# Performance work log

Measured on AMD Instinct MI355X. Metric: run time of the kernel, lower is better.

## Reference

```python
import jax, jax.numpy as jnp
import numpy as np

B, C, H, W = 4, 256, 64, 64
CH = C // 2


def setup_inputs() -> dict:
    key = jax.random.key(0)
    ks = jax.random.split(key, 8)
    s_in = 1.0 / np.sqrt(C)  # conv2d default init scale (fan_in = C for 1x1)
    return {
        "a": jax.random.normal(ks[0], (B, C, H, W), dtype=jnp.float32),
        "p": jax.random.normal(ks[1], (B, C, H, W), dtype=jnp.float32),
        "Wq": jax.random.uniform(ks[2], (CH, C), jnp.float32, -s_in, s_in),
        "bq": jax.random.uniform(ks[3], (CH,), jnp.float32, -s_in, s_in),
        "Wk": jax.random.uniform(ks[4], (CH, C), jnp.float32, -s_in, s_in),
        "bk": jax.random.uniform(ks[5], (CH,), jnp.float32, -s_in, s_in),
        "Wv": jax.random.uniform(ks[6], (C, C), jnp.float32, -s_in, s_in),
        "bv": jax.random.uniform(ks[7], (C,), jnp.float32, -s_in, s_in),
    }


def reference(a, p, Wq, bq, Wk, bk, Wv, bv):
    b, c, h, w = a.shape
    hw = h * w
    # 1x1 convs == per-pixel channel matmuls; flatten spatial dims to hw
    Q = jnp.einsum('oc,bchw->bohw', Wq, a).reshape(b, -1, hw) + bq[None, :, None]   # [B, C/2, HW]
    K = jnp.einsum('oc,bchw->bohw', Wk, p).reshape(b, -1, hw) + bk[None, :, None]   # [B, C/2, HW]
    V = jnp.einsum('oc,bchw->bohw', Wv, p).reshape(b, -1, hw) + bv[None, :, None]   # [B, C,   HW]
    # attn[b,m,n] = softmax_n( Q[:, :, m] . K[:, :, n] )
    attn = jax.nn.softmax(jnp.einsum('bcm,bcn->bmn', Q, K), axis=-1)                # [B, HW, HW]
    # out[b,c,m] = sum_n V[b,c,n] * attn[b,m,n]  (V @ attn^T)
    out = jnp.einsum('bcn,bmn->bcm', V, attn).reshape(b, c, h, w)
    return out + a
```

## Files before the change

kernel.cpp:

```cpp
#include <hip/hip_runtime.h>
#include <stdint.h>

#define B_ 4
#define C_ 256
#define CH_ 128
#define HW_ 4096
#define L2E 1.44269504f
#define SHIFT_L2 14.4269504f

typedef __bf16 bf16;
typedef __bf16 v8bf __attribute__((ext_vector_type(8)));
typedef __bf16 v4bf __attribute__((ext_vector_type(4)));
typedef float v4f __attribute__((ext_vector_type(4)));
struct f4 { float x, y, z, w; };
struct f2 { float x, y; };

#define GAS __attribute__((address_space(1)))
#define LAS __attribute__((address_space(3)))

__device__ __forceinline__ void async_copy16(const void* gptr, void* lptr) {
  __builtin_amdgcn_global_load_lds((GAS void*)gptr, (LAS void*)lptr, 16, 0, 0);
}

__global__ __launch_bounds__(512)
void proj_kernel(const float* __restrict__ a, const float* __restrict__ p,
                 const float* __restrict__ Wq, const float* __restrict__ bq,
                 const float* __restrict__ Wk, const float* __restrict__ bk,
                 const float* __restrict__ Wv, const float* __restrict__ bv,
                 bf16* __restrict__ Qt, bf16* __restrict__ Kt, bf16* __restrict__ Vn)
{
  __shared__ bf16 Xt[64 * 272];
  __shared__ bf16 Ds[9216];

  const int t = threadIdx.x;
  const int lane = t & 63;
  const int w = t >> 6;
  const int l15 = lane & 15;
  const int q = lane >> 4;

  const int s0 = blockIdx.x * 64;
  const int b = blockIdx.y;
  const int z = blockIdx.z;

  const float* X = (z == 0) ? a : p;
  const float* Xb = X + ((size_t)b * C_) * HW_;
  #pragma unroll
  for (int j = 0; j < 8; ++j) {
    int linear = t + 512 * j;
    int s = (linear & 31) * 2;
    int cp = linear >> 5;
    f2 x0 = *(const f2*)&Xb[(size_t)(2 * cp) * HW_ + s0 + s];
    f2 x1 = *(const f2*)&Xb[(size_t)(2 * cp + 1) * HW_ + s0 + s];
    unsigned short u00 = __builtin_bit_cast(unsigned short, (bf16)x0.x);
    unsigned short u01 = __builtin_bit_cast(unsigned short, (bf16)x0.y);
    unsigned short u10 = __builtin_bit_cast(unsigned short, (bf16)x1.x);
    unsigned short u11 = __builtin_bit_cast(unsigned short, (bf16)x1.y);
    *(unsigned int*)&Xt[(s + 0) * 272 + 2 * cp] = (unsigned int)u00 | ((unsigned int)u10 << 16);
    *(unsigned int*)&Xt[(s + 1) * 272 + 2 * cp] = (unsigned int)u01 | ((unsigned int)u11 << 16);
  }

  __syncthreads();

  const int npass = (z == 0) ? 1 : 3;
  for (int pp = 0; pp < npass; ++pp) {
    const float* W; const float* bias;
    if (z == 0)      { W = Wq; bias = bq; }
    else if (pp == 0){ W = Wk; bias = bk; }
    else             { W = Wv + (size_t)(pp - 1) * 128 * C_; bias = bv + (pp - 1) * 128; }

    v8bf Af[8];
    const float* Wrow = W + (size_t)(16 * w + l15) * C_;
    #pragma unroll
    for (int kk = 0; kk < 8; ++kk) {
      f4 f0 = *(const f4*)&Wrow[kk * 32 + q * 8];
      f4 f1 = *(const f4*)&Wrow[kk * 32 + q * 8 + 4];
      v8bf f;
      f[0] = (bf16)f0.x; f[1] = (bf16)f0.y; f[2] = (bf16)f0.z; f[3] = (bf16)f0.w;
      f[4] = (bf16)f1.x; f[5] = (bf16)f1.y; f[6] = (bf16)f1.z; f[7] = (bf16)f1.w;
      Af[kk] = f;
    }

    v4f acc[4];
    #pragma unroll
    for (int ns = 0; ns < 4; ++ns) { v4f zz = {0.f, 0.f, 0.f, 0.f}; acc[ns] = zz; }
    #pragma unroll
    for (int ns = 0; ns < 4; ++ns)
      #pragma unroll
      for (int kk = 0; kk < 8; ++kk) {
        v8bf Bf = *(const v8bf*)&Xt[(16 * ns + l15) * 272 + kk * 32 + q * 8];
        acc[ns] = __builtin_amdgcn_mfma_f32_16x16x32_bf16(Af[kk], Bf, acc[ns], 0, 0, 0);
      }

    if (z == 0 || pp == 0) {
      #pragma unroll
      for (int ns = 0; ns < 4; ++ns)
        #pragma unroll
        for (int r = 0; r < 4; ++r)
          Ds[(16 * ns + l15) * 144 + 16 * w + 4 * q + r] =
              (bf16)(acc[ns][r] + bias[16 * w + 4 * q + r]);
      __syncthreads();
      bf16* dst = (z == 0) ? Qt : Kt;
      #pragma unroll
      for (int i = 0; i < 2; ++i) {
        int idx = t + 512 * i;
        int s = idx >> 4, ch = (idx & 15) * 8;
        *(v8bf*)&dst[((size_t)b * HW_ + s0 + s) * CH_ + ch] = *(const v8bf*)&Ds[s * 144 + ch];
      }
    } else {
      int o0 = (pp - 1) * 128;
      #pragma unroll
      for (int ns = 0; ns < 4; ++ns)
        #pragma unroll
        for (int r = 0; r < 4; ++r) {
          int pos = 32 * (ns >> 1) + 8 * (l15 >> 2) + 4 * (ns & 1) + (l15 & 3);
          Ds[(16 * w + 4 * q + r) * 72 + pos] =
              (bf16)(acc[ns][r] + bias[16 * w + 4 * q + r]);
        }
      __syncthreads();
      #pragma unroll
      for (int i = 0; i < 2; ++i) {
        int idx = t + 512 * i;
        int o = idx >> 3, ch = (idx & 7) * 8;
        *(v8bf*)&Vn[((size_t)b * C_ + o0 + o) * HW_ + s0 + ch] = *(const v8bf*)&Ds[o * 72 + ch];
      }
    }
    if (pp + 1 < npass) __syncthreads();
  }
}

#define LDS_V 16640
#define TSTRIDE 52
#define TREGION 13312
#define LDS_TOTAL 53248

__global__ __launch_bounds__(256, 2)
void attn_kernel(const bf16* __restrict__ Qt, const bf16* __restrict__ Kt,
                 const bf16* __restrict__ Vn, const float* __restrict__ a,
                 float* __restrict__ out, bf16* __restrict__ Op,
                 float* __restrict__ Ls, int nsplit)
{
  extern __shared__ char smem[];
  const int t = threadIdx.x;
  const int lane = t & 63;
  const int w = t >> 6;
  const int l15 = lane & 15;
  const int q = lane >> 4;
  const int b = blockIdx.y;
  const int sp = blockIdx.z;
  const int m0 = blockIdx.x * 128;

  v8bf Qf[2][4];
  #pragma unroll
  for (int s = 0; s < 2; ++s) {
    const bf16* qrow = Qt + ((size_t)b * HW_ + m0 + 32 * w + 16 * s + l15) * CH_;
    #pragma unroll
    for (int kk = 0; kk < 4; ++kk)
      Qf[s][kk] = *(const v8bf*)&qrow[kk * 32 + q * 8];
  }

  v4f O[2][16];
  #pragma unroll
  for (int s = 0; s < 2; ++s)
    #pragma unroll
    for (int cs = 0; cs < 16; ++cs) { v4f zz = {0.f, 0.f, 0.f, 0.f}; O[s][cs] = zz; }
  float lsum[2] = {0.f, 0.f};

  const bf16* Kb = Kt + (size_t)b * HW_ * CH_;
  const bf16* Vb = Vn + (size_t)b * C_ * HW_;

  const int NT = 64 / nsplit;
  const int t0 = sp * NT;

  auto stageK = [&](int n0) {
    #pragma unroll
    for (int j = 0; j < 4; ++j) {
      int i = 4 * j + w;
      async_copy16(Kb + ((size_t)(n0 + i + 16 * q)) * CH_ + l15 * 8, smem + i * 1040);
    }
  };
  auto stageV = [&](int n0) {
    #pragma unroll
    for (int j = 0; j < 8; ++j) {
      int i = 4 * j + w;
      async_copy16(Vb + ((size_t)(i + 32 * (lane >> 3))) * HW_ + n0 + (lane & 7) * 8,
                   smem + LDS_V + i * 1040);
    }
  };

  stageK(t0 * 64);
  stageV(t0 * 64);
  __syncthreads();

  for (int nt = 0; nt < NT; ++nt) {
    int n0 = (t0 + nt) * 64;

    v4f St[4][2];
    #pragma unroll
    for (int sub = 0; sub < 4; ++sub)
      #pragma unroll
      for (int s = 0; s < 2; ++s) { v4f zz = {0.f, 0.f, 0.f, 0.f}; St[sub][s] = zz; }
    #pragma unroll
    for (int sub = 0; sub < 4; ++sub)
      #pragma unroll
      for (int kk = 0; kk < 4; ++kk) {
        v8bf Kf = *(const v8bf*)(smem + l15 * 1040 + sub * 256 + kk * 64 + q * 16);
        St[sub][0] = __builtin_amdgcn_mfma_f32_16x16x32_bf16(Kf, Qf[0][kk], St[sub][0], 0, 0, 0);
        St[sub][1] = __builtin_amdgcn_mfma_f32_16x16x32_bf16(Kf, Qf[1][kk], St[sub][1], 0, 0, 0);
      }

    __syncthreads();
    if (nt + 1 < NT) stageK(n0 + 64);

    v8bf Pf[2][2];
    #pragma unroll
    for (int s = 0; s < 2; ++s) {
      float ls = 0.f;
      #pragma unroll
      for (int kk = 0; kk < 2; ++kk)
        #pragma unroll
        for (int a2 = 0; a2 < 2; ++a2)
          #pragma unroll
          for (int r = 0; r < 4; ++r) {
            float pv = exp2f(St[2 * kk + a2][s][r] * L2E - SHIFT_L2);
            Pf[s][kk][4 * a2 + r] = (bf16)pv;
            ls += pv;
          }
      lsum[s] += ls;
    }

    #pragma unroll
    for (int cs = 0; cs < 16; ++cs)
      #pragma unroll
      for (int kk = 0; kk < 2; ++kk) {
        v8bf Vf = *(const v8bf*)(smem + LDS_V +
                                 (16 * (cs & 1) + l15) * 1040 + (cs >> 1) * 128 + kk * 64 + q * 16);
        O[0][cs] = __builtin_amdgcn_mfma_f32_16x16x32_bf16(Pf[0][kk], Vf, O[0][cs], 0, 0, 0);
        O[1][cs] = __builtin_amdgcn_mfma_f32_16x16x32_bf16(Pf[1][kk], Vf, O[1][cs], 0, 0, 0);
      }

    __syncthreads();
    if (nt + 1 < NT) stageV(n0 + 64);
  }

  float lfin[2];
  #pragma unroll
  for (int s = 0; s < 2; ++s) {
    float l = lsum[s];
    l += __shfl_xor(l, 16);
    l += __shfl_xor(l, 32);
    lfin[s] = l;
  }

  if (nsplit > 1 && lane < 16) {
    #pragma unroll
    for (int s = 0; s < 2; ++s)
      Ls[((size_t)sp * B_ + b) * HW_ + m0 + 32 * w + 16 * s + lane] = lfin[s];
  }

  float linv[2][4];
  #pragma unroll
  for (int s = 0; s < 2; ++s)
    #pragma unroll
    for (int r = 0; r < 4; ++r)
      linv[s][r] = (nsplit == 1) ? 1.0f / __shfl(lfin[s], 4 * q + r) : 1.0f;

  bf16* T = (bf16*)smem;
  for (int round = 0; round < 2; ++round) {
    __syncthreads();
    if ((w >> 1) == round) {
      bf16* Tw = T + (w & 1) * TREGION;
      #pragma unroll
      for (int s = 0; s < 2; ++s)
        #pragma unroll
        for (int cs = 0; cs < 16; ++cs) {
          v4bf pp4;
          #pragma unroll
          for (int r = 0; r < 4; ++r) pp4[r] = (bf16)(O[s][cs][r] * linv[s][r]);
          *(v4bf*)&Tw[(16 * cs + l15) * TSTRIDE + 16 * s + 4 * q] = pp4;
        }
    }
    __syncthreads();
    #pragma unroll
    for (int it = 0; it < 8; ++it) {
      int idx = t + 256 * it;
      int tt = idx >> 10;
      int c = (idx >> 2) & 255;
      int mc = idx & 3;
      int wavew = round * 2 + tt;
      int mg = m0 + 32 * wavew + mc * 8;
      const bf16* Trow = &T[tt * TREGION + c * TSTRIDE + mc * 8];
      v4bf lo = *(const v4bf*)&Trow[0];
      v4bf hi = *(const v4bf*)&Trow[4];
      if (nsplit == 1) {
        size_t gi = ((size_t)b * C_ + c) * HW_ + mg;
        #pragma unroll
        for (int j2 = 0; j2 < 4; ++j2) out[gi + j2] = (float)lo[j2] + a[gi + j2];
        #pragma unroll
        for (int j2 = 0; j2 < 4; ++j2) out[gi + 4 + j2] = (float)hi[j2] + a[gi + 4 + j2];
      } else {
        size_t gi = (((size_t)sp * B_ + b) * C_ + c) * HW_ + mg;
        v8bf val;
        #pragma unroll
        for (int j2 = 0; j2 < 4; ++j2) { val[j2] = lo[j2]; val[4 + j2] = hi[j2]; }
        *(v8bf*)&Op[gi] = val;
      }
    }
  }
}

__global__ __launch_bounds__(256)
void combine_kernel(const bf16* __restrict__ Op, const float* __restrict__ Ls,
                    const float* __restrict__ a, float* __restrict__ out, int nsplit)
{
  int idx = blockIdx.x * 256 + threadIdx.x;
  int m4 = (idx & (HW_ / 4 - 1)) * 4;
  int bc = idx >> 10;
  int b = bc >> 8;

  float a0 = 0.f, a1 = 0.f, a2 = 0.f, a3 = 0.f;
  float L0 = 0.f, L1 = 0.f, L2 = 0.f, L3 = 0.f;
  for (int s = 0; s < nsplit; ++s) {
    v4bf o = *(const v4bf*)&Op[((size_t)s * B_ * C_ + bc) * HW_ + m4];
    f4 lp = *(const f4*)&Ls[((size_t)s * B_ + b) * HW_ + m4];
    a0 += (float)o[0]; a1 += (float)o[1]; a2 += (float)o[2]; a3 += (float)o[3];
    L0 += lp.x; L1 += lp.y; L2 += lp.z; L3 += lp.w;
  }
  f4 av = *(const f4*)&a[(size_t)bc * HW_ + m4];
  f4 ov;
  ov.x = a0 / L0 + av.x;
  ov.y = a1 / L1 + av.y;
  ov.z = a2 / L2 + av.z;
  ov.w = a3 / L3 + av.w;
  *(f4*)&out[(size_t)bc * HW_ + m4] = ov;
}

extern "C" void kernel_launch(void* const* d_in, const int* in_sizes, int n_in,
                              void* d_out, int out_size, void* d_ws, size_t ws_size,
                              hipStream_t stream) {
  const float* a  = (const float*)d_in[0];
  const float* p  = (const float*)d_in[1];
  const float* Wq = (const float*)d_in[2];
  const float* bq = (const float*)d_in[3];
  const float* Wk = (const float*)d_in[4];
  const float* bk = (const float*)d_in[5];
  const float* Wv = (const float*)d_in[6];
  const float* bv = (const float*)d_in[7];
  float* out = (float*)d_out;

  bf16* Qt = (bf16*)d_ws;
  bf16* Kt = Qt + (size_t)B_ * HW_ * CH_;
  bf16* Vn = Kt + (size_t)B_ * HW_ * CH_;

  const size_t proj_bytes = 16777216ull;
  const size_t part_bytes = (size_t)B_ * C_ * HW_ * 2;
  const size_t stat_bytes = (size_t)B_ * HW_ * 4;
  auto need = [&](int S) { return proj_bytes + (size_t)S * (part_bytes + stat_bytes); };

  int S;
  if      (ws_size >= need(4)) S = 4;
  else if (ws_size >= need(2)) S = 2;
  else                         S = 1;

  bf16* Op = (bf16*)((char*)d_ws + proj_bytes);
  float* Ls = (float*)((char*)d_ws + proj_bytes + (size_t)S * part_bytes);

  dim3 pg(HW_ / 64, B_, 2);
  proj_kernel<<<pg, 512, 0, stream>>>(a, p, Wq, bq, Wk, bk, Wv, bv, Qt, Kt, Vn);

  dim3 ag(HW_ / 128, B_, S);
  attn_kernel<<<ag, 256, LDS_TOTAL, stream>>>(Qt, Kt, Vn, a, out, Op, Ls, S);

  if (S > 1) {
    int nblk = (B_ * C_ * HW_ / 4) / 256;
    combine_kernel<<<nblk, 256, 0, stream>>>(Op, Ls, a, out, S);
  }
}
```

Measured before the change: 178.3 us.

## Split projection grid per weight and fuse split-K combine into attention via atomics

The projection kernel now launches four z-slices (Q, K, V-lo, V-hi) instead of two. This removes the serial three-pass loop on the p-side blocks and adds parallelism at the cost of loading the p tile twice more. The separate combine kernel is removed: each attention block increments an atomic counter, and the last split block to finish for a row tile reduces the partials and writes the output. A memset of the counters is added each launch. This trades a kernel launch and a full-grid pass for a serialized tail in the last-arriving blocks.

```diff
diff --git a/kernel.cpp b/kernel.cpp
--- a/kernel.cpp
+++ b/kernel.cpp
@@ -43,6 +43,11 @@
   const int z = blockIdx.z;
 
   const float* X = (z == 0) ? a : p;
+  const float* W; const float* bias;
+  if (z == 0)      { W = Wq; bias = bq; }
+  else if (z == 1) { W = Wk; bias = bk; }
+  else             { W = Wv + (size_t)(z - 2) * 128 * C_; bias = bv + (z - 2) * 128; }
+
   const float* Xb = X + ((size_t)b * C_) * HW_;
   #pragma unroll
   for (int j = 0; j < 8; ++j) {
@@ -59,72 +64,63 @@
     *(unsigned int*)&Xt[(s + 1) * 272 + 2 * cp] = (unsigned int)u01 | ((unsigned int)u11 << 16);
   }
 
+  v8bf Af[8];
+  const float* Wrow = W + (size_t)(16 * w + l15) * C_;
+  #pragma unroll
+  for (int kk = 0; kk < 8; ++kk) {
+    f4 f0 = *(const f4*)&Wrow[kk * 32 + q * 8];
+    f4 f1 = *(const f4*)&Wrow[kk * 32 + q * 8 + 4];
+    v8bf f;
+    f[0] = (bf16)f0.x; f[1] = (bf16)f0.y; f[2] = (bf16)f0.z; f[3] = (bf16)f0.w;
+    f[4] = (bf16)f1.x; f[5] = (bf16)f1.y; f[6] = (bf16)f1.z; f[7] = (bf16)f1.w;
+    Af[kk] = f;
+  }
+
   __syncthreads();
 
-  const int npass = (z == 0) ? 1 : 3;
-  for (int pp = 0; pp < npass; ++pp) {
-    const float* W; const float* bias;
-    if (z == 0)      { W = Wq; bias = bq; }
-    else if (pp == 0){ W = Wk; bias = bk; }
-    else             { W = Wv + (size_t)(pp - 1) * 128 * C_; bias = bv + (pp - 1) * 128; }
-
-    v8bf Af[8];
-    const float* Wrow = W + (size_t)(16 * w + l15) * C_;
+  v4f acc[4];
+  #pragma unroll
+  for (int ns = 0; ns < 4; ++ns) { v4f zz = {0.f, 0.f, 0.f, 0.f}; acc[ns] = zz; }
+  #pragma unroll
+  for (int ns = 0; ns < 4; ++ns)
     #pragma unroll
     for (int kk = 0; kk < 8; ++kk) {
-      f4 f0 = *(const f4*)&Wrow[kk * 32 + q * 8];
-      f4 f1 = *(const f4*)&Wrow[kk * 32 + q * 8 + 4];
-      v8bf f;
-      f[0] = (bf16)f0.x; f[1] = (bf16)f0.y; f[2] = (bf16)f0.z; f[3] = (bf16)f0.w;
-      f[4] = (bf16)f1.x; f[5] = (bf16)f1.y; f[6] = (bf16)f1.z; f[7] = (bf16)f1.w;
-      Af[kk] = f;
-    }
-
-    v4f acc[4];
-    #pragma unroll
-    for (int ns = 0; ns < 4; ++ns) { v4f zz = {0.f, 0.f, 0.f, 0.f}; acc[ns] = zz; }
+      v8bf Bf = *(const v8bf*)&Xt[(16 * ns + l15) * 272 + kk * 32 + q * 8];
+      acc[ns] = __builtin_amdgcn_mfma_f32_16x16x32_bf16(Af[kk], Bf, acc[ns], 0, 0, 0);
+    }
+
+  if (z < 2) {
     #pragma unroll
     for (int ns = 0; ns < 4; ++ns)
       #pragma unroll
-      for (int kk = 0; kk < 8; ++kk) {
-        v8bf Bf = *(const v8bf*)&Xt[(16 * ns + l15) * 272 + kk * 32 + q * 8];
-        acc[ns] = __builtin_amdgcn_mfma_f32_16x16x32_bf16(Af[kk], Bf, acc[ns], 0, 0, 0);
-      }
-
-    if (z == 0 || pp == 0) {
-      #pragma unroll
-      for (int ns = 0; ns < 4; ++ns)
-        #pragma unroll
-        for (int r = 0; r < 4; ++r)
-          Ds[(16 * ns + l15) * 144 + 16 * w + 4 * q + r] =
-              (bf16)(acc[ns][r] + bias[16 * w + 4 * q + r]);
-      __syncthreads();
-      bf16* dst = (z == 0) ? Qt : Kt;
-      #pragma unroll
-      for (int i = 0; i < 2; ++i) {
-        int idx = t + 512 * i;
-        int s = idx >> 4, ch = (idx & 15) * 8;
-        *(v8bf*)&dst[((size_t)b * HW_ + s0 + s) * CH_ + ch] = *(const v8bf*)&Ds[s * 144 + ch];
-      }
-    } else {
-      int o0 = (pp - 1) * 128;
-      #pragma unroll
-      for (int ns = 0; ns < 4; ++ns)
-        #pragma unroll
-        for (int r = 0; r < 4; ++r) {
-          int pos = 32 * (ns >> 1) + 8 * (l15 >> 2) + 4 * (ns & 1) + (l15 & 3);
-          Ds[(16 * w + 4 * q + r) * 72 + pos] =
-              (bf16)(acc[ns][r] + bias[16 * w + 4 * q + r]);
-        }
-      __syncthreads();
-      #pragma unroll
-      for (int i = 0; i < 2; ++i) {
-        int idx = t + 512 * i;
-        int o = idx >> 3, ch = (idx & 7) * 8;
-        *(v8bf*)&Vn[((size_t)b * C_ + o0 + o) * HW_ + s0 + ch] = *(const v8bf*)&Ds[o * 72 + ch];
-      }
-    }
-    if (pp + 1 < npass) __syncthreads();
+      for (int r = 0; r < 4; ++r)
+        Ds[(16 * ns + l15) * 144 + 16 * w + 4 * q + r] =
+            (bf16)(acc[ns][r] + bias[16 * w + 4 * q + r]);
+    __syncthreads();
+    bf16* dst = (z == 0) ? Qt : Kt;
+    #pragma unroll
+    for (int i = 0; i < 2; ++i) {
+      int idx = t + 512 * i;
+      int s = idx >> 4, ch = (idx & 15) * 8;
+      *(v8bf*)&dst[((size_t)b * HW_ + s0 + s) * CH_ + ch] = *(const v8bf*)&Ds[s * 144 + ch];
+    }
+  } else {
+    int o0 = (z - 2) * 128;
+    #pragma unroll
+    for (int ns = 0; ns < 4; ++ns)
+      #pragma unroll
+      for (int r = 0; r < 4; ++r) {
+        int pos = 32 * (ns >> 1) + 8 * (l15 >> 2) + 4 * (ns & 1) + (l15 & 3);
+        Ds[(16 * w + 4 * q + r) * 72 + pos] =
+            (bf16)(acc[ns][r] + bias[16 * w + 4 * q + r]);
+      }
+    __syncthreads();
+    #pragma unroll
+    for (int i = 0; i < 2; ++i) {
+      int idx = t + 512 * i;
+      int o = idx >> 3, ch = (idx & 7) * 8;
+      *(v8bf*)&Vn[((size_t)b * C_ + o0 + o) * HW_ + s0 + ch] = *(const v8bf*)&Ds[o * 72 + ch];
+    }
   }
 }
 
@@ -137,7 +133,7 @@
 void attn_kernel(const bf16* __restrict__ Qt, const bf16* __restrict__ Kt,
                  const bf16* __restrict__ Vn, const float* __restrict__ a,
                  float* __restrict__ out, bf16* __restrict__ Op,
-                 float* __restrict__ Ls, int nsplit)
+                 float* __restrict__ Ls, int* __restrict__ cnt, int nsplit)
 {
   extern __shared__ char smem[];
   const int t = threadIdx.x;
@@ -306,32 +302,47 @@
       }
     }
   }
-}
-
-__global__ __launch_bounds__(256)
-void combine_kernel(const bf16* __restrict__ Op, const float* __restrict__ Ls,
-                    const float* __restrict__ a, float* __restrict__ out, int nsplit)
-{
-  int idx = blockIdx.x * 256 + threadIdx.x;
-  int m4 = (idx & (HW_ / 4 - 1)) * 4;
-  int bc = idx >> 10;
-  int b = bc >> 8;
-
-  float a0 = 0.f, a1 = 0.f, a2 = 0.f, a3 = 0.f;
-  float L0 = 0.f, L1 = 0.f, L2 = 0.f, L3 = 0.f;
-  for (int s = 0; s < nsplit; ++s) {
-    v4bf o = *(const v4bf*)&Op[((size_t)s * B_ * C_ + bc) * HW_ + m4];
-    f4 lp = *(const f4*)&Ls[((size_t)s * B_ + b) * HW_ + m4];
-    a0 += (float)o[0]; a1 += (float)o[1]; a2 += (float)o[2]; a3 += (float)o[3];
-    L0 += lp.x; L1 += lp.y; L2 += lp.z; L3 += lp.w;
-  }
-  f4 av = *(const f4*)&a[(size_t)bc * HW_ + m4];
-  f4 ov;
-  ov.x = a0 / L0 + av.x;
-  ov.y = a1 / L1 + av.y;
-  ov.z = a2 / L2 + av.z;
-  ov.w = a3 / L3 + av.w;
-  *(f4*)&out[(size_t)bc * HW_ + m4] = ov;
+
+  if (nsplit > 1) {
+    __threadfence();
+    __shared__ int lastFlag;
+    if (t == 0) {
+      int old = atomicAdd(&cnt[b * (HW_ / 128) + blockIdx.x], 1);
+      lastFlag = (old == nsplit - 1) ? 1 : 0;
+    }
+    __syncthreads();
+    if (lastFlag) {
+      __threadfence();
+      const int mc = t & 31;
+      const int m4 = m0 + mc * 4;
+      float Li[4];
+      {
+        float L0 = 0.f, L1 = 0.f, L2 = 0.f, L3 = 0.f;
+        for (int s = 0; s < nsplit; ++s) {
+          f4 lp = *(const f4*)&Ls[((size_t)s * B_ + b) * HW_ + m4];
+          L0 += lp.x; L1 += lp.y; L2 += lp.z; L3 += lp.w;
+        }
+        Li[0] = 1.0f / L0; Li[1] = 1.0f / L1; Li[2] = 1.0f / L2; Li[3] = 1.0f / L3;
+      }
+      const int cbase = t >> 5;
+      for (int it = 0; it < 32; ++it) {
+        int c = cbase + 8 * it;
+        float a0 = 0.f, a1 = 0.f, a2 = 0.f, a3 = 0.f;
+        for (int s = 0; s < nsplit; ++s) {
+          v4bf o = *(const v4bf*)&Op[(((size_t)s * B_ + b) * C_ + c) * HW_ + m4];
+          a0 += (float)o[0]; a1 += (float)o[1]; a2 += (float)o[2]; a3 += (float)o[3];
+        }
+        size_t gi = ((size_t)b * C_ + c) * HW_ + m4;
+        f4 av = *(const f4*)&a[gi];
+        f4 ov;
+        ov.x = a0 * Li[0] + av.x;
+        ov.y = a1 * Li[1] + av.y;
+        ov.z = a2 * Li[2] + av.z;
+        ov.w = a3 * Li[3] + av.w;
+        *(f4*)&out[gi] = ov;
+      }
+    }
+  }
 }
 
 extern "C" void kernel_launch(void* const* d_in, const int* in_sizes, int n_in,
@@ -354,24 +365,25 @@
   const size_t proj_bytes = 16777216ull;
   const size_t part_bytes = (size_t)B_ * C_ * HW_ * 2;
   const size_t stat_bytes = (size_t)B_ * HW_ * 4;
-  auto need = [&](int S) { return proj_bytes + (size_t)S * (part_bytes + stat_bytes); };
+  const size_t cnt_bytes  = 512;
+  auto need = [&](int S) {
+    return proj_bytes + (size_t)S * (part_bytes + stat_bytes) + cnt_bytes;
+  };
 
   int S;
   if      (ws_size >= need(4)) S = 4;
   else if (ws_size >= need(2)) S = 2;
   else                         S = 1;
 
-  bf16* Op = (bf16*)((char*)d_ws + proj_bytes);
+  bf16* Op  = (bf16*)((char*)d_ws + proj_bytes);
   float* Ls = (float*)((char*)d_ws + proj_bytes + (size_t)S * part_bytes);
-
-  dim3 pg(HW_ / 64, B_, 2);
+  int* cnt  = (int*)((char*)d_ws + proj_bytes + (size_t)S * (part_bytes + stat_bytes));
+
+  dim3 pg(HW_ / 64, B_, 4);
   proj_kernel<<<pg, 512, 0, stream>>>(a, p, Wq, bq, Wk, bk, Wv, bv, Qt, Kt, Vn);
 
+  if (S > 1) hipMemsetAsync(cnt, 0, cnt_bytes, stream);
+
   dim3 ag(HW_ / 128, B_, S);
-  attn_kernel<<<ag, 256, LDS_TOTAL, stream>>>(Qt, Kt, Vn, a, out, Op, Ls, S);
-
-  if (S > 1) {
-    int nblk = (B_ * C_ * HW_ / 4) / 256;
-    combine_kernel<<<nblk, 256, 0, stream>>>(Op, Ls, a, out, S);
-  }
+  attn_kernel<<<ag, 256, LDS_TOTAL, stream>>>(Qt, Kt, Vn, a, out, Op, Ls, cnt, S);
 }
```

Result: slower. 409.9 us (+129.8%).
